# Optimization experiments

Hardware: AMD Instinct MI355X
Metric: run time of the kernel (lower is better)

Reference implementation:

```python
import jax, jax.numpy as jnp
import numpy as np

N_EMBD = 1024
HEAD_SIZE = 64
B, T = 4, 4096


def setup_inputs() -> dict:
    key = jax.random.key(0)
    kx, kk, kq, kv = jax.random.split(key, 4)
    s = 1.0 / np.sqrt(N_EMBD)
    return {
        "x": jax.random.normal(kx, (B, T, N_EMBD), dtype=jnp.float32),
        "Wk": jax.random.normal(kk, (N_EMBD, HEAD_SIZE), dtype=jnp.float32) * s,
        "Wq": jax.random.normal(kq, (N_EMBD, HEAD_SIZE), dtype=jnp.float32) * s,
        "Wv": jax.random.normal(kv, (N_EMBD, HEAD_SIZE), dtype=jnp.float32) * s,
    }


def reference(x, Wk, Wq, Wv):
    Bb, Tt, C = x.shape
    k = x @ Wk  # [B,T,H]
    q = x @ Wq
    v = x @ Wv
    # scores scaled by C**-0.5 where C = n_embd (as in the original module)
    w = jnp.einsum('bth,bsh->bts', q, k) * (C ** -0.5)  # [B,T,T]
    causal = jnp.tril(jnp.ones((Tt, Tt), dtype=bool))
    w = jnp.where(causal, w, -jnp.inf)
    w = jax.nn.softmax(w, axis=-1)
    # dropout prob is 0.0 (eval) -> identity
    out = jnp.einsum('bts,bsh->bth', w, v)  # [B,T,H]
    return out
```

## Files before the change

kernel.cpp:

```cpp
#include <hip/hip_runtime.h>


#define BSZ 4
#define TSZ 4096
#define CSZ 1024
#define MSZ (BSZ * TSZ)
#define NS 8
#define QT 128
#define NQT (TSZ / QT)

typedef _Float16 half8 __attribute__((ext_vector_type(8)));
typedef _Float16 half4 __attribute__((ext_vector_type(4)));
typedef float f32x4 __attribute__((ext_vector_type(4)));

#define MFMA(a, b, c) __builtin_amdgcn_mfma_f32_16x16x32_f16((a), (b), (c), 0, 0, 0)
#define QSCALE 0.04508422002778011f

__device__ __forceinline__ int kimg(int r, int h) {
    return r * 64 + ((((h >> 3) ^ (r & 7))) << 3) + (h & 7);
}
__device__ __forceinline__ int vimg(int kk, int h) {
    int p = (kk & 15) * 4 + (kk >> 4);
    return h * 64 + ((((p >> 3) ^ (h & 7))) << 3) + (p & 7);
}

__device__ __forceinline__ void glds16(const _Float16* g, _Float16* l) {
    __builtin_amdgcn_global_load_lds(
        (const __attribute__((address_space(1))) void*)g,
        (__attribute__((address_space(3))) void*)l, 16, 0, 0);
}

__global__ __launch_bounds__(192) void wconv(const float* __restrict__ Wk,
                                             const float* __restrict__ Wq,
                                             const float* __restrict__ Wv,
                                             _Float16* __restrict__ Wt) {
    int kk = blockIdx.x;
    int n = threadIdx.x;
    const float* W = (n < 64) ? Wk : ((n < 128) ? Wq : Wv);
    float v = W[kk * 64 + (n & 63)];
    if (n >= 64 && n < 128) v *= QSCALE;
    Wt[(size_t)n * 1024 + kk] = (_Float16)v;
}

__global__ __launch_bounds__(256) void qkv_proj(const float* __restrict__ x,
                                                const _Float16* __restrict__ Wt,
                                                _Float16* __restrict__ qbf,
                                                _Float16* __restrict__ kbs,
                                                _Float16* __restrict__ vts) {
    __shared__ _Float16 xt[2][32 * 128];

    int tid = threadIdx.x;
    int wave = tid >> 6, lane = tid & 63;
    int quad = lane >> 4, l16 = lane & 15;
    int row0 = blockIdx.x * 32;

    f32x4 acc[6];
#pragma unroll
    for (int i = 0; i < 6; i++) acc[i] = (f32x4){0.f, 0.f, 0.f, 0.f};

    int sr = tid >> 3;
    int sc = tid & 7;
    const float* xrow = x + (size_t)(row0 + sr) * CSZ + sc * 16;

    f32x4 p[4];
#pragma unroll
    for (int i = 0; i < 4; i++) p[i] = *(const f32x4*)(xrow + i * 4);

    int cur = 0;
    for (int kc = 0; kc < CSZ; kc += 128, cur ^= 1) {
        {
            _Float16 tmp[16] __attribute__((aligned(16)));
#pragma unroll
            for (int i = 0; i < 16; i++) tmp[i] = (_Float16)p[i >> 2][i & 3];
            *(half8*)&xt[cur][sr * 128 + ((sc * 2) ^ (sr & 7)) * 8] =
                *(half8*)tmp;
            *(half8*)&xt[cur][sr * 128 + ((sc * 2 + 1) ^ (sr & 7)) * 8] =
                *(half8*)(tmp + 8);
        }
        __syncthreads();
        if (kc + 128 < CSZ) {
#pragma unroll
            for (int i = 0; i < 4; i++)
                p[i] = *(const f32x4*)(xrow + kc + 128 + i * 4);
        }
#pragma unroll
        for (int ss = 0; ss < 4; ss++) {
            half8 a0 = *(half8*)&xt[cur][l16 * 128 +
                                         ((ss * 4 + quad) ^ (l16 & 7)) * 8];
            half8 a1 = *(half8*)&xt[cur][(16 + l16) * 128 +
                                         ((ss * 4 + quad) ^ (l16 & 7)) * 8];
#pragma unroll
            for (int j = 0; j < 3; j++) {
                int ct = wave * 3 + j;
                half8 bb = *(const half8*)&Wt[(size_t)(ct * 16 + l16) * CSZ +
                                              kc + ss * 32 + quad * 8];
                acc[j * 2 + 0] = MFMA(a0, bb, acc[j * 2 + 0]);
                acc[j * 2 + 1] = MFMA(a1, bb, acc[j * 2 + 1]);
            }
        }
    }

#pragma unroll
    for (int j = 0; j < 3; j++) {
        int ct = wave * 3 + j;
        int kind = ct >> 2;
        int col = (ct & 3) * 16 + l16;
#pragma unroll
        for (int m = 0; m < 2; m++) {
#pragma unroll
            for (int r = 0; r < 4; r++) {
                int row = row0 + m * 16 + quad * 4 + r;
                _Float16 val = (_Float16)acc[j * 2 + m][r];
                if (kind == 0) {
                    kbs[((size_t)(row >> 6)) * 4096 + kimg(row & 63, col)] = val;
                } else if (kind == 1) {
                    qbf[(size_t)row * 64 + col] = val;
                } else {
                    vts[((size_t)(row >> 6)) * 4096 + vimg(row & 63, col)] = val;
                }
            }
        }
    }
}

__global__ __launch_bounds__(256) void attn_partial(
    const _Float16* __restrict__ qbf, const _Float16* __restrict__ kbs,
    const _Float16* __restrict__ vts, _Float16* __restrict__ opart,
    float* __restrict__ ml) {
    __shared__ _Float16 kt[2][4096];
    __shared__ _Float16 vt[2][4096];
    __shared__ _Float16 pt[QT * 64];

    int tid = threadIdx.x;
    int wave = tid >> 6, lane = tid & 63;
    int quad = lane >> 4, l16 = lane & 15;
    int s = blockIdx.x & (NS - 1);
    int qt = (blockIdx.x >> 3) & (NQT - 1);
    int b = blockIdx.x >> 8;
    int nt = 2 * (qt + 1);
    int lo = s * nt / NS, hi = (s + 1) * nt / NS;
    int part = (b * NQT + qt) * NS + s;

    if (lo >= hi) {
        if (tid < QT) ml[part * QT + tid] = 0.f;
        return;
    }

    const _Float16* qb = qbf + (size_t)b * TSZ * 64;
    const _Float16* kbs_b = kbs + (size_t)b * 64 * 4096;
    const _Float16* vts_b = vts + (size_t)b * 64 * 4096;

    int qrow = qt * QT + wave * 32;
    half8 aq[2][2];
#pragma unroll
    for (int st = 0; st < 2; st++)
#pragma unroll
        for (int ss = 0; ss < 2; ss++)
            aq[st][ss] = *(const half8*)&qb[(qrow + st * 16 + l16) * 64 +
                                            ss * 32 + quad * 8];

    f32x4 o[2][4];
    float l_acc[2][4];
#pragma unroll
    for (int st = 0; st < 2; st++)
#pragma unroll
        for (int ct = 0; ct < 4; ct++) {
            o[st][ct] = (f32x4){0.f, 0.f, 0.f, 0.f};
            l_acc[st][ct] = 0.f;
        }

    int soff = wave * 512 + lane * 8;

    {
        const _Float16* ks = kbs_b + (size_t)lo * 4096 + soff;
        const _Float16* vs = vts_b + (size_t)lo * 4096 + soff;
        glds16(ks, &kt[0][soff]);
        glds16(ks + 2048, &kt[0][2048 + soff]);
        glds16(vs, &vt[0][soff]);
        glds16(vs + 2048, &vt[0][2048 + soff]);
    }

    int cur = 0;
    for (int kti = lo; kti < hi; kti++, cur ^= 1) {
        __syncthreads();
        if (kti + 1 < hi) {
            const _Float16* ks = kbs_b + (size_t)(kti + 1) * 4096 + soff;
            const _Float16* vs = vts_b + (size_t)(kti + 1) * 4096 + soff;
            glds16(ks, &kt[cur ^ 1][soff]);
            glds16(ks + 2048, &kt[cur ^ 1][2048 + soff]);
            glds16(vs, &vt[cur ^ 1][soff]);
            glds16(vs + 2048, &vt[cur ^ 1][2048 + soff]);
        }

        f32x4 sacc[2][4];
#pragma unroll
        for (int st = 0; st < 2; st++)
#pragma unroll
            for (int ct = 0; ct < 4; ct++)
                sacc[st][ct] = (f32x4){0.f, 0.f, 0.f, 0.f};
#pragma unroll
        for (int ss = 0; ss < 2; ss++) {
#pragma unroll
            for (int ct = 0; ct < 4; ct++) {
                half8 bb = *(half8*)&kt[cur][(ct * 16 + l16) * 64 +
                                             ((ss * 4 + quad) ^ (l16 & 7)) * 8];
                sacc[0][ct] = MFMA(aq[0][ss], bb, sacc[0][ct]);
                sacc[1][ct] = MFMA(aq[1][ss], bb, sacc[1][ct]);
            }
        }

        bool diag = (kti >= 2 * qt);
#pragma unroll
        for (int st = 0; st < 2; st++) {
#pragma unroll
            for (int r = 0; r < 4; r++) {
                int lrow = wave * 32 + st * 16 + quad * 4 + r;
                float pv[4];
#pragma unroll
                for (int ct = 0; ct < 4; ct++) {
                    float e = exp2f(sacc[st][ct][r]);
                    if (diag) {
                        int key = kti * 64 + ct * 16 + l16;
                        if (key > qt * QT + lrow) e = 0.f;
                    }
                    pv[ct] = e;
                }
                l_acc[st][r] += pv[0] + pv[1] + pv[2] + pv[3];
                half4 hp;
#pragma unroll
                for (int ct = 0; ct < 4; ct++) hp[ct] = (_Float16)pv[ct];
                int chunk = (l16 >> 1) ^ (lrow & 7);
                *(half4*)&pt[lrow * 64 + chunk * 8 + (l16 & 1) * 4] = hp;
            }
        }

#pragma unroll
        for (int ss = 0; ss < 2; ss++) {
            half8 ap0 = *(half8*)&pt[(wave * 32 + l16) * 64 +
                                     ((ss * 4 + quad) ^ (l16 & 7)) * 8];
            half8 ap1 = *(half8*)&pt[(wave * 32 + 16 + l16) * 64 +
                                     ((ss * 4 + quad) ^ (l16 & 7)) * 8];
#pragma unroll
            for (int ct = 0; ct < 4; ct++) {
                half8 bv = *(half8*)&vt[cur][(ct * 16 + l16) * 64 +
                                             ((ss * 4 + quad) ^ (l16 & 7)) * 8];
                o[0][ct] = MFMA(ap0, bv, o[0][ct]);
                o[1][ct] = MFMA(ap1, bv, o[1][ct]);
            }
        }
    }

#pragma unroll
    for (int off = 1; off < 16; off <<= 1) {
#pragma unroll
        for (int st = 0; st < 2; st++)
#pragma unroll
            for (int r = 0; r < 4; r++)
                l_acc[st][r] += __shfl_xor(l_acc[st][r], off);
    }

    _Float16* op = opart + (size_t)part * (QT * 64);
#pragma unroll
    for (int st = 0; st < 2; st++) {
#pragma unroll
        for (int r = 0; r < 4; r++) {
            int lrow = wave * 32 + st * 16 + quad * 4 + r;
            float li = l_acc[st][r];
            float inv = li > 0.f ? 1.f / li : 0.f;
#pragma unroll
            for (int ct = 0; ct < 4; ct++)
                op[lrow * 64 + ct * 16 + l16] = (_Float16)(o[st][ct][r] * inv);
            if (l16 == 0) ml[part * QT + lrow] = li;
        }
    }
}

__global__ __launch_bounds__(256) void combine(
    const _Float16* __restrict__ opart, const float* __restrict__ ml,
    float* __restrict__ out) {
    int tid = threadIdx.x;
    int row = blockIdx.x * 32 + (tid >> 3);
    int seg = (tid & 7) * 8;
    int b = row >> 12;
    int qt = (row >> 7) & (NQT - 1);
    int prow = row & (QT - 1);
    int pbase = (b * NQT + qt) * NS;

    float acc[8];
#pragma unroll
    for (int i = 0; i < 8; i++) acc[i] = 0.f;
    float lsum = 0.f;
#pragma unroll
    for (int s = 0; s < NS; s++) {
        float l = ml[(pbase + s) * QT + prow];
        lsum += l;
        half8 h = *(const half8*)&opart[(size_t)(pbase + s) * (QT * 64) +
                                        prow * 64 + seg];
#pragma unroll
        for (int i = 0; i < 8; i++) acc[i] += l * (float)h[i];
    }
    float inv = 1.f / lsum;
    float* ob = out + (size_t)row * 64 + seg;
#pragma unroll
    for (int i = 0; i < 8; i++) ob[i] = acc[i] * inv;
}

extern "C" void kernel_launch(void* const* d_in, const int* in_sizes, int n_in,
                              void* d_out, int out_size, void* d_ws,
                              size_t ws_size, hipStream_t stream) {
    (void)in_sizes; (void)n_in; (void)out_size; (void)ws_size;
    const float* x = (const float*)d_in[0];
    const float* Wk = (const float*)d_in[1];
    const float* Wq = (const float*)d_in[2];
    const float* Wv = (const float*)d_in[3];

    _Float16* Wt = (_Float16*)d_ws;
    _Float16* qbf = Wt + 192 * 1024;
    _Float16* kbs = qbf + (size_t)MSZ * 64;
    _Float16* vts = kbs + (size_t)MSZ * 64;
    _Float16* opart = vts + (size_t)MSZ * 64;
    float* ml = (float*)(opart + (size_t)BSZ * NQT * NS * QT * 64);

    wconv<<<1024, 192, 0, stream>>>(Wk, Wq, Wv, Wt);
    qkv_proj<<<MSZ / 32, 256, 0, stream>>>(x, Wt, qbf, kbs, vts);
    attn_partial<<<BSZ * NQT * NS, 256, 0, stream>>>(qbf, kbs, vts, opart, ml);
    combine<<<MSZ / 32, 256, 0, stream>>>(opart, ml, (float*)d_out);
}
```

Measured before the change: 162.3 us.

## Split-K QKV projection with LDS reduction; read K/V directly from global in attention

The weight conversion now writes a K-step-blocked fp16 layout with vector stores from 32 blocks. The projection kernel splits the 1024-wide reduction across four waves, each computing all 12 column tiles, and combines partial sums through LDS float atomics before writing plain row-major K/Q and a transposed V. The attention kernel drops the async global-to-LDS double-buffered K/V staging and instead loads MFMA operands straight from global/L2, with a padded P tile in LDS replacing the XOR swizzle. This simplifies the layouts and removes the barriers in the attention loop, but it gives up LDS reuse of K/V across waves and adds LDS atomic contention in the projection.

```diff
diff --git a/kernel.cpp b/kernel.cpp
--- a/kernel.cpp
+++ b/kernel.cpp
@@ -10,126 +10,118 @@
 #define NQT (TSZ / QT)
 
 typedef _Float16 half8 __attribute__((ext_vector_type(8)));
-typedef _Float16 half4 __attribute__((ext_vector_type(4)));
 typedef float f32x4 __attribute__((ext_vector_type(4)));
 
 #define MFMA(a, b, c) __builtin_amdgcn_mfma_f32_16x16x32_f16((a), (b), (c), 0, 0, 0)
 #define QSCALE 0.04508422002778011f
-
-__device__ __forceinline__ int kimg(int r, int h) {
-    return r * 64 + ((((h >> 3) ^ (r & 7))) << 3) + (h & 7);
-}
-__device__ __forceinline__ int vimg(int kk, int h) {
-    int p = (kk & 15) * 4 + (kk >> 4);
-    return h * 64 + ((((p >> 3) ^ (h & 7))) << 3) + (p & 7);
-}
-
-__device__ __forceinline__ void glds16(const _Float16* g, _Float16* l) {
-    __builtin_amdgcn_global_load_lds(
-        (const __attribute__((address_space(1))) void*)g,
-        (__attribute__((address_space(3))) void*)l, 16, 0, 0);
-}
 
 __global__ __launch_bounds__(192) void wconv(const float* __restrict__ Wk,
                                              const float* __restrict__ Wq,
                                              const float* __restrict__ Wv,
-                                             _Float16* __restrict__ Wt) {
-    int kk = blockIdx.x;
+                                             _Float16* __restrict__ Wt2) {
+    int kstep = blockIdx.x;
     int n = threadIdx.x;
     const float* W = (n < 64) ? Wk : ((n < 128) ? Wq : Wv);
-    float v = W[kk * 64 + (n & 63)];
-    if (n >= 64 && n < 128) v *= QSCALE;
-    Wt[(size_t)n * 1024 + kk] = (_Float16)v;
+    float sc = (n >= 64 && n < 128) ? QSCALE : 1.0f;
+    _Float16 h[32] __attribute__((aligned(16)));
+#pragma unroll
+    for (int ki = 0; ki < 32; ki++)
+        h[ki] = (_Float16)(W[(kstep * 32 + ki) * 64 + (n & 63)] * sc);
+    _Float16* dst = Wt2 + ((size_t)kstep * 192 + n) * 32;
+#pragma unroll
+    for (int i = 0; i < 4; i++) *(half8*)(dst + i * 8) = *(half8*)(h + i * 8);
 }
 
 __global__ __launch_bounds__(256) void qkv_proj(const float* __restrict__ x,
-                                                const _Float16* __restrict__ Wt,
+                                                const _Float16* __restrict__ Wt2,
                                                 _Float16* __restrict__ qbf,
-                                                _Float16* __restrict__ kbs,
-                                                _Float16* __restrict__ vts) {
-    __shared__ _Float16 xt[2][32 * 128];
+                                                _Float16* __restrict__ kbf,
+                                                _Float16* __restrict__ vtb) {
+    __shared__ float red[32 * 196];
 
     int tid = threadIdx.x;
     int wave = tid >> 6, lane = tid & 63;
     int quad = lane >> 4, l16 = lane & 15;
     int row0 = blockIdx.x * 32;
 
-    f32x4 acc[6];
-#pragma unroll
-    for (int i = 0; i < 6; i++) acc[i] = (f32x4){0.f, 0.f, 0.f, 0.f};
-
-    int sr = tid >> 3;
-    int sc = tid & 7;
-    const float* xrow = x + (size_t)(row0 + sr) * CSZ + sc * 16;
-
-    f32x4 p[4];
-#pragma unroll
-    for (int i = 0; i < 4; i++) p[i] = *(const f32x4*)(xrow + i * 4);
-
-    int cur = 0;
-    for (int kc = 0; kc < CSZ; kc += 128, cur ^= 1) {
-        {
-            _Float16 tmp[16] __attribute__((aligned(16)));
-#pragma unroll
-            for (int i = 0; i < 16; i++) tmp[i] = (_Float16)p[i >> 2][i & 3];
-            *(half8*)&xt[cur][sr * 128 + ((sc * 2) ^ (sr & 7)) * 8] =
-                *(half8*)tmp;
-            *(half8*)&xt[cur][sr * 128 + ((sc * 2 + 1) ^ (sr & 7)) * 8] =
-                *(half8*)(tmp + 8);
-        }
-        __syncthreads();
-        if (kc + 128 < CSZ) {
-#pragma unroll
-            for (int i = 0; i < 4; i++)
-                p[i] = *(const f32x4*)(xrow + kc + 128 + i * 4);
-        }
-#pragma unroll
-        for (int ss = 0; ss < 4; ss++) {
-            half8 a0 = *(half8*)&xt[cur][l16 * 128 +
-                                         ((ss * 4 + quad) ^ (l16 & 7)) * 8];
-            half8 a1 = *(half8*)&xt[cur][(16 + l16) * 128 +
-                                         ((ss * 4 + quad) ^ (l16 & 7)) * 8];
-#pragma unroll
-            for (int j = 0; j < 3; j++) {
-                int ct = wave * 3 + j;
-                half8 bb = *(const half8*)&Wt[(size_t)(ct * 16 + l16) * CSZ +
-                                              kc + ss * 32 + quad * 8];
-                acc[j * 2 + 0] = MFMA(a0, bb, acc[j * 2 + 0]);
-                acc[j * 2 + 1] = MFMA(a1, bb, acc[j * 2 + 1]);
-            }
-        }
-    }
-
-#pragma unroll
-    for (int j = 0; j < 3; j++) {
-        int ct = wave * 3 + j;
-        int kind = ct >> 2;
-        int col = (ct & 3) * 16 + l16;
+    for (int i = tid; i < 32 * 196; i += 256) red[i] = 0.f;
+
+    f32x4 acc[12][2];
+#pragma unroll
+    for (int ct = 0; ct < 12; ct++)
+#pragma unroll
+        for (int m = 0; m < 2; m++) acc[ct][m] = (f32x4){0.f, 0.f, 0.f, 0.f};
+
+    const float* x0 = x + (size_t)(row0 + l16) * CSZ + wave * 256 + quad * 8;
+    const float* x1 = x0 + 16 * CSZ;
+
+#pragma unroll
+    for (int k8 = 0; k8 < 8; k8++) {
+        int gk = wave * 8 + k8;
+        f32x4 a0 = *(const f32x4*)(x0 + k8 * 32);
+        f32x4 a0b = *(const f32x4*)(x0 + k8 * 32 + 4);
+        f32x4 a1 = *(const f32x4*)(x1 + k8 * 32);
+        f32x4 a1b = *(const f32x4*)(x1 + k8 * 32 + 4);
+        half8 ha0, ha1;
+#pragma unroll
+        for (int i = 0; i < 4; i++) {
+            ha0[i] = (_Float16)a0[i];
+            ha0[4 + i] = (_Float16)a0b[i];
+            ha1[i] = (_Float16)a1[i];
+            ha1[4 + i] = (_Float16)a1b[i];
+        }
+        const _Float16* wp = Wt2 + ((size_t)gk * 192 + l16) * 32 + quad * 8;
+#pragma unroll
+        for (int ct = 0; ct < 12; ct++) {
+            half8 bb = *(const half8*)(wp + ct * 16 * 32);
+            acc[ct][0] = MFMA(ha0, bb, acc[ct][0]);
+            acc[ct][1] = MFMA(ha1, bb, acc[ct][1]);
+        }
+    }
+
+    __syncthreads();
+#pragma unroll
+    for (int ct = 0; ct < 12; ct++) {
 #pragma unroll
         for (int m = 0; m < 2; m++) {
 #pragma unroll
             for (int r = 0; r < 4; r++) {
-                int row = row0 + m * 16 + quad * 4 + r;
-                _Float16 val = (_Float16)acc[j * 2 + m][r];
-                if (kind == 0) {
-                    kbs[((size_t)(row >> 6)) * 4096 + kimg(row & 63, col)] = val;
-                } else if (kind == 1) {
-                    qbf[(size_t)row * 64 + col] = val;
-                } else {
-                    vts[((size_t)(row >> 6)) * 4096 + vimg(row & 63, col)] = val;
-                }
-            }
-        }
+                atomicAdd(&red[(m * 16 + quad * 4 + r) * 196 + ct * 16 + l16],
+                          acc[ct][m][r]);
+            }
+        }
+    }
+    __syncthreads();
+
+    {
+        int row = tid >> 3, c8 = (tid & 7) * 8;
+        _Float16 hk[8] __attribute__((aligned(16)));
+        _Float16 hq[8] __attribute__((aligned(16)));
+#pragma unroll
+        for (int i = 0; i < 8; i++) {
+            hk[i] = (_Float16)red[row * 196 + c8 + i];
+            hq[i] = (_Float16)red[row * 196 + 64 + c8 + i];
+        }
+        *(half8*)&kbf[(size_t)(row0 + row) * 64 + c8] = *(half8*)hk;
+        *(half8*)&qbf[(size_t)(row0 + row) * 64 + c8] = *(half8*)hq;
+    }
+    {
+        int h = tid >> 2, rg = tid & 3;
+        _Float16 hv[8] __attribute__((aligned(16)));
+#pragma unroll
+        for (int i = 0; i < 8; i++)
+            hv[i] = (_Float16)red[(rg * 8 + i) * 196 + 128 + h];
+        size_t bb = (size_t)(row0 >> 12);
+        *(half8*)&vtb[(bb * 64 + h) * TSZ + (row0 & 4095) + rg * 8] =
+            *(half8*)hv;
     }
 }
 
 __global__ __launch_bounds__(256) void attn_partial(
-    const _Float16* __restrict__ qbf, const _Float16* __restrict__ kbs,
-    const _Float16* __restrict__ vts, _Float16* __restrict__ opart,
+    const _Float16* __restrict__ qbf, const _Float16* __restrict__ kbf,
+    const _Float16* __restrict__ vtb, _Float16* __restrict__ opart,
     float* __restrict__ ml) {
-    __shared__ _Float16 kt[2][4096];
-    __shared__ _Float16 vt[2][4096];
-    __shared__ _Float16 pt[QT * 64];
+    __shared__ _Float16 pt[QT * 72];
 
     int tid = threadIdx.x;
     int wave = tid >> 6, lane = tid & 63;
@@ -147,8 +139,8 @@
     }
 
     const _Float16* qb = qbf + (size_t)b * TSZ * 64;
-    const _Float16* kbs_b = kbs + (size_t)b * 64 * 4096;
-    const _Float16* vts_b = vts + (size_t)b * 64 * 4096;
+    const _Float16* kb = kbf + (size_t)b * TSZ * 64;
+    const _Float16* vb = vtb + (size_t)b * 64 * TSZ;
 
     int qrow = qt * QT + wave * 32;
     half8 aq[2][2];
@@ -156,7 +148,7 @@
     for (int st = 0; st < 2; st++)
 #pragma unroll
         for (int ss = 0; ss < 2; ss++)
-            aq[st][ss] = *(const half8*)&qb[(qrow + st * 16 + l16) * 64 +
+            aq[st][ss] = *(const half8*)&qb[(size_t)(qrow + st * 16 + l16) * 64 +
                                             ss * 32 + quad * 8];
 
     f32x4 o[2][4];
@@ -169,29 +161,7 @@
             l_acc[st][ct] = 0.f;
         }
 
-    int soff = wave * 512 + lane * 8;
-
-    {
-        const _Float16* ks = kbs_b + (size_t)lo * 4096 + soff;
-        const _Float16* vs = vts_b + (size_t)lo * 4096 + soff;
-        glds16(ks, &kt[0][soff]);
-        glds16(ks + 2048, &kt[0][2048 + soff]);
-        glds16(vs, &vt[0][soff]);
-        glds16(vs + 2048, &vt[0][2048 + soff]);
-    }
-
-    int cur = 0;
-    for (int kti = lo; kti < hi; kti++, cur ^= 1) {
-        __syncthreads();
-        if (kti + 1 < hi) {
-            const _Float16* ks = kbs_b + (size_t)(kti + 1) * 4096 + soff;
-            const _Float16* vs = vts_b + (size_t)(kti + 1) * 4096 + soff;
-            glds16(ks, &kt[cur ^ 1][soff]);
-            glds16(ks + 2048, &kt[cur ^ 1][2048 + soff]);
-            glds16(vs, &vt[cur ^ 1][soff]);
-            glds16(vs + 2048, &vt[cur ^ 1][2048 + soff]);
-        }
-
+    for (int kti = lo; kti < hi; kti++) {
         f32x4 sacc[2][4];
 #pragma unroll
         for (int st = 0; st < 2; st++)
@@ -202,8 +172,9 @@
         for (int ss = 0; ss < 2; ss++) {
 #pragma unroll
             for (int ct = 0; ct < 4; ct++) {
-                half8 bb = *(half8*)&kt[cur][(ct * 16 + l16) * 64 +
-                                             ((ss * 4 + quad) ^ (l16 & 7)) * 8];
+                half8 bb = *(const half8*)&kb[(size_t)(kti * 64 + ct * 16 + l16) *
+                                                  64 +
+                                              ss * 32 + quad * 8];
                 sacc[0][ct] = MFMA(aq[0][ss], bb, sacc[0][ct]);
                 sacc[1][ct] = MFMA(aq[1][ss], bb, sacc[1][ct]);
             }
@@ -226,24 +197,21 @@
                     pv[ct] = e;
                 }
                 l_acc[st][r] += pv[0] + pv[1] + pv[2] + pv[3];
-                half4 hp;
-#pragma unroll
-                for (int ct = 0; ct < 4; ct++) hp[ct] = (_Float16)pv[ct];
-                int chunk = (l16 >> 1) ^ (lrow & 7);
-                *(half4*)&pt[lrow * 64 + chunk * 8 + (l16 & 1) * 4] = hp;
+#pragma unroll
+                for (int ct = 0; ct < 4; ct++)
+                    pt[lrow * 72 + ct * 16 + l16] = (_Float16)pv[ct];
             }
         }
 
 #pragma unroll
         for (int ss = 0; ss < 2; ss++) {
-            half8 ap0 = *(half8*)&pt[(wave * 32 + l16) * 64 +
-                                     ((ss * 4 + quad) ^ (l16 & 7)) * 8];
-            half8 ap1 = *(half8*)&pt[(wave * 32 + 16 + l16) * 64 +
-                                     ((ss * 4 + quad) ^ (l16 & 7)) * 8];
+            half8 ap0 = *(half8*)&pt[(wave * 32 + l16) * 72 + ss * 32 + quad * 8];
+            half8 ap1 = *(half8*)&pt[(wave * 32 + 16 + l16) * 72 + ss * 32 +
+                                     quad * 8];
 #pragma unroll
             for (int ct = 0; ct < 4; ct++) {
-                half8 bv = *(half8*)&vt[cur][(ct * 16 + l16) * 64 +
-                                             ((ss * 4 + quad) ^ (l16 & 7)) * 8];
+                half8 bv = *(const half8*)&vb[(size_t)(ct * 16 + l16) * TSZ +
+                                              kti * 64 + ss * 32 + quad * 8];
                 o[0][ct] = MFMA(ap0, bv, o[0][ct]);
                 o[1][ct] = MFMA(ap1, bv, o[1][ct]);
             }
@@ -314,15 +282,15 @@
     const float* Wq = (const float*)d_in[2];
     const float* Wv = (const float*)d_in[3];
 
-    _Float16* Wt = (_Float16*)d_ws;
-    _Float16* qbf = Wt + 192 * 1024;
-    _Float16* kbs = qbf + (size_t)MSZ * 64;
-    _Float16* vts = kbs + (size_t)MSZ * 64;
-    _Float16* opart = vts + (size_t)MSZ * 64;
+    _Float16* Wt2 = (_Float16*)d_ws;
+    _Float16* qbf = Wt2 + 192 * 1024;
+    _Float16* kbf = qbf + (size_t)MSZ * 64;
+    _Float16* vtb = kbf + (size_t)MSZ * 64;
+    _Float16* opart = vtb + (size_t)MSZ * 64;
     float* ml = (float*)(opart + (size_t)BSZ * NQT * NS * QT * 64);
 
-    wconv<<<1024, 192, 0, stream>>>(Wk, Wq, Wv, Wt);
-    qkv_proj<<<MSZ / 32, 256, 0, stream>>>(x, Wt, qbf, kbs, vts);
-    attn_partial<<<BSZ * NQT * NS, 256, 0, stream>>>(qbf, kbs, vts, opart, ml);
+    wconv<<<32, 192, 0, stream>>>(Wk, Wq, Wv, Wt2);
+    qkv_proj<<<MSZ / 32, 256, 0, stream>>>(x, Wt2, qbf, kbf, vtb);
+    attn_partial<<<BSZ * NQT * NS, 256, 0, stream>>>(qbf, kbf, vtb, opart, ml);
     combine<<<MSZ / 32, 256, 0, stream>>>(opart, ml, (float*)d_out);
 }
```

Result: slower. 248.8 us (+53.3%).
